# Kernel tuning notes

Measured on AMD Instinct MI355X. Metric: run time of the kernel, lower is better.

Reference implementation:

```python
import jax, jax.numpy as jnp
import numpy as np

B, T, D = 32, 512, 384
DUR_MAX = 8          # durations drawn from [0, DUR_MAX)
MAX_LEN = T * (DUR_MAX - 1)  # 3584, static pad length (= target_mel_len)


def setup_inputs() -> dict:
    key = jax.random.key(0)
    kx, kd = jax.random.split(key)
    x = jax.random.normal(kx, (B, T, D), dtype=jnp.float32)
    duration_target = jax.random.randint(kd, (B, T), 0, DUR_MAX, dtype=jnp.int64)
    return {"x": x, "duration_target": duration_target, "target_mel_len": MAX_LEN}


def reference(x, duration_target, target_mel_len):
    # Effective duration: original does vec.expand(max(int(d), 1), -1),
    # so zero durations still produce one frame.
    eff = jnp.maximum(duration_target, 1)          # [B, T]
    cum = jnp.cumsum(eff, axis=1)                   # [B, T] exclusive upper bounds
    mel_len = cum[:, -1]                            # [B]
    L = int(target_mel_len)                         # static pad length
    frames = jnp.arange(L)                          # [L]
    # frame j belongs to phoneme i where cum[i-1] <= j < cum[i]
    idx = jax.vmap(lambda c: jnp.searchsorted(c, frames, side="right"))(cum)  # [B, L]
    idx = jnp.minimum(idx, x.shape[1] - 1)          # clamp padded region
    out = jnp.take_along_axis(x, idx[:, :, None], axis=1)  # [B, L, D]
    mask = frames[None, :] < mel_len[:, None]       # [B, L]
    out = out * mask[:, :, None].astype(out.dtype)  # zero padding like F.pad
    return out, mel_len.astype(jnp.int64)
```

## Files before the change

### kernel.cpp

```cpp
#include <hip/hip_runtime.h>


#define B_DIM 32
#define T_DIM 512
#define D_DIM 384
#define L_DIM 3584
#define VEC_PER_ROW 96
#define PAIRS_PER_BATCH (L_DIM * VEC_PER_ROW / 2)
#define GATHER_BLOCK 256
#define BLOCKS_PER_BATCH (PAIRS_PER_BATCH / GATHER_BLOCK)
#define GATHER_BLOCKS (BLOCKS_PER_BATCH * B_DIM)

typedef float f32x4 __attribute__((ext_vector_type(4)));

__global__ void __launch_bounds__(T_DIM)
lr_build_map(const int* __restrict__ dur, int* __restrict__ idx_map,
             float* __restrict__ mel_out) {
    const int b    = blockIdx.x;
    const int t    = threadIdx.x;
    const int lane = t & 63;
    const int wv   = t >> 6;

    int d = dur[b * T_DIM + t];
    int e = d > 1 ? d : 1;

    int val = e;
    #pragma unroll
    for (int off = 1; off < 64; off <<= 1) {
        int n = __shfl_up(val, off, 64);
        if (lane >= off) val += n;
    }

    __shared__ int wsum[8];
    if (lane == 63) wsum[wv] = val;
    __syncthreads();

    int base = 0, tot = 0;
    #pragma unroll
    for (int i = 0; i < 8; ++i) {
        int s = wsum[i];
        tot += s;
        if (i < wv) base += s;
    }

    const int cum   = val + base;
    const int mel   = tot;
    const int start = cum - e;

    int* map_b = idx_map + b * L_DIM;
    for (int k = 0; k < e; ++k)
        map_b[start + k] = t;

    for (int f = mel + t; f < L_DIM; f += T_DIM)
        map_b[f] = -1;

    if (t == 0)
        mel_out[b] = (float)mel;
}

__global__ void __launch_bounds__(GATHER_BLOCK)
lr_gather(const f32x4* __restrict__ x, const int* __restrict__ idx_map,
          f32x4* __restrict__ out) {
    const int bid = blockIdx.x;
    const int blk = (bid & 7) * (GATHER_BLOCKS / 8) + (bid >> 3);

    const int b    = blk / BLOCKS_PER_BATCH;
    const int pblk = blk - b * BLOCKS_PER_BATCH;
    const int p    = pblk * GATHER_BLOCK + threadIdx.x;
    const int v0   = p << 1;
    const int f    = v0 / VEC_PER_ROW;
    const int w    = v0 - f * VEC_PER_ROW;

    const int idx = idx_map[b * L_DIM + f];
    f32x4 a = (f32x4)0.f;
    f32x4 c = (f32x4)0.f;
    if (idx >= 0) {
        const f32x4* row = x + ((b * T_DIM + idx) * VEC_PER_ROW);
        a = row[w];
        c = row[w + 1];
    }
    f32x4* o = out + (size_t)(b * L_DIM + f) * VEC_PER_ROW + w;
    __builtin_nontemporal_store(a, o);
    __builtin_nontemporal_store(c, o + 1);
}

extern "C" void kernel_launch(void* const* d_in, const int* in_sizes, int n_in,
                              void* d_out, int out_size, void* d_ws, size_t ws_size,
                              hipStream_t stream) {
    const float* x   = (const float*)d_in[0];
    const int*   dur = (const int*)d_in[1];

    int*   idx_map = (int*)d_ws;
    float* out     = (float*)d_out;
    float* mel_out = out + (size_t)B_DIM * L_DIM * D_DIM;

    lr_build_map<<<dim3(B_DIM), dim3(T_DIM), 0, stream>>>(dur, idx_map, mel_out);

    lr_gather<<<dim3(GATHER_BLOCKS), dim3(GATHER_BLOCK), 0, stream>>>(
        (const f32x4*)x, idx_map, (f32x4*)out);
}
```

Measured before the change: 221.8 us.

## Replace per-frame gather with per-phoneme scatter from LDS-staged rows

The scan kernel now only writes cumulative durations instead of building a full frame-to-phoneme index map. The write kernel has each block load 8 source rows of x into LDS once and write out every frame those rows cover, finding the owning row with seven comparisons. Separate blocks zero-fill the padded tail past mel_len. This removes the index-map writes and reads and the repeated global reads of x, at the cost of uneven per-block work and no longer using nontemporal stores.

```diff
diff --git a/kernel.cpp b/kernel.cpp
--- a/kernel.cpp
+++ b/kernel.cpp
@@ -5,17 +5,21 @@
 #define T_DIM 512
 #define D_DIM 384
 #define L_DIM 3584
-#define VEC_PER_ROW 96
-#define PAIRS_PER_BATCH (L_DIM * VEC_PER_ROW / 2)
-#define GATHER_BLOCK 256
-#define BLOCKS_PER_BATCH (PAIRS_PER_BATCH / GATHER_BLOCK)
-#define GATHER_BLOCKS (BLOCKS_PER_BATCH * B_DIM)
+#define VEC 96
+#define RPB 8
+#define CHUNKS (T_DIM / RPB)
+#define SCATTER_BLOCKS (B_DIM * CHUNKS)
+#define TAIL_F0 T_DIM
+#define TAIL_FPB 256
+#define TAIL_CHUNKS ((L_DIM - TAIL_F0) / TAIL_FPB)
+#define TAIL_BLOCKS (B_DIM * TAIL_CHUNKS)
+#define TOTAL_BLOCKS (SCATTER_BLOCKS + TAIL_BLOCKS)
 
 typedef float f32x4 __attribute__((ext_vector_type(4)));
 
 __global__ void __launch_bounds__(T_DIM)
-lr_build_map(const int* __restrict__ dur, int* __restrict__ idx_map,
-             float* __restrict__ mel_out) {
+lr_scan(const int* __restrict__ dur, int* __restrict__ cum_out,
+        float* __restrict__ mel_out) {
     const int b    = blockIdx.x;
     const int t    = threadIdx.x;
     const int lane = t & 63;
@@ -43,45 +47,64 @@
         if (i < wv) base += s;
     }
 
-    const int cum   = val + base;
-    const int mel   = tot;
-    const int start = cum - e;
-
-    int* map_b = idx_map + b * L_DIM;
-    for (int k = 0; k < e; ++k)
-        map_b[start + k] = t;
-
-    for (int f = mel + t; f < L_DIM; f += T_DIM)
-        map_b[f] = -1;
-
-    if (t == 0)
-        mel_out[b] = (float)mel;
+    cum_out[b * T_DIM + t] = val + base;
+    if (t == 0) mel_out[b] = (float)tot;
 }
 
-__global__ void __launch_bounds__(GATHER_BLOCK)
-lr_gather(const f32x4* __restrict__ x, const int* __restrict__ idx_map,
-          f32x4* __restrict__ out) {
-    const int bid = blockIdx.x;
-    const int blk = (bid & 7) * (GATHER_BLOCKS / 8) + (bid >> 3);
+__global__ void __launch_bounds__(256)
+lr_write(const f32x4* __restrict__ x, const int* __restrict__ cum,
+         f32x4* __restrict__ out) {
+    const int blk = blockIdx.x;
+    const int tid = threadIdx.x;
 
-    const int b    = blk / BLOCKS_PER_BATCH;
-    const int pblk = blk - b * BLOCKS_PER_BATCH;
-    const int p    = pblk * GATHER_BLOCK + threadIdx.x;
-    const int v0   = p << 1;
-    const int f    = v0 / VEC_PER_ROW;
-    const int w    = v0 - f * VEC_PER_ROW;
+    if (blk < SCATTER_BLOCKS) {
+        const int b  = blk / CHUNKS;
+        const int c  = blk - b * CHUNKS;
+        const int r0 = c * RPB;
 
-    const int idx = idx_map[b * L_DIM + f];
-    f32x4 a = (f32x4)0.f;
-    f32x4 c = (f32x4)0.f;
-    if (idx >= 0) {
-        const f32x4* row = x + ((b * T_DIM + idx) * VEC_PER_ROW);
-        a = row[w];
-        c = row[w + 1];
+        __shared__ f32x4 lx[RPB * VEC];
+        __shared__ int   scum[RPB + 1];
+
+        if (tid <= RPB) {
+            int r = r0 - 1 + tid;
+            scum[tid] = (r < 0) ? 0 : cum[b * T_DIM + r];
+        }
+        const f32x4* xb = x + (b * T_DIM + r0) * VEC;
+        #pragma unroll
+        for (int i = 0; i < (RPB * VEC) / 256; ++i)
+            lx[tid + i * 256] = xb[tid + i * 256];
+        __syncthreads();
+
+        const int f0 = scum[0];
+        const int s1 = scum[1], s2 = scum[2], s3 = scum[3], s4 = scum[4],
+                  s5 = scum[5], s6 = scum[6], s7 = scum[7];
+        const int span = (scum[RPB] - f0) * VEC;
+
+        f32x4* ob = out + (size_t)(b * L_DIM + f0) * VEC;
+        for (int v = tid; v < span; v += 256) {
+            const int fr = v / VEC;
+            const int w  = v - fr * VEC;
+            const int fa = f0 + fr;
+            int r = (fa >= s1) + (fa >= s2) + (fa >= s3) + (fa >= s4)
+                  + (fa >= s5) + (fa >= s6) + (fa >= s7);
+            ob[v] = lx[r * VEC + w];
+        }
+    } else {
+        const int tb = blk - SCATTER_BLOCKS;
+        const int b  = tb / TAIL_CHUNKS;
+        const int c  = tb - b * TAIL_CHUNKS;
+        const int mel = cum[b * T_DIM + T_DIM - 1];
+        const int fs = TAIL_F0 + c * TAIL_FPB;
+        const int lo = fs > mel ? fs : mel;
+        const int hi = fs + TAIL_FPB;
+        if (lo < hi) {
+            const f32x4 z = (f32x4)0.f;
+            f32x4* ob = out + (size_t)(b * L_DIM + lo) * VEC;
+            const int span = (hi - lo) * VEC;
+            for (int v = tid; v < span; v += 256)
+                ob[v] = z;
+        }
     }
-    f32x4* o = out + (size_t)(b * L_DIM + f) * VEC_PER_ROW + w;
-    __builtin_nontemporal_store(a, o);
-    __builtin_nontemporal_store(c, o + 1);
 }
 
 extern "C" void kernel_launch(void* const* d_in, const int* in_sizes, int n_in,
@@ -90,12 +113,12 @@
     const float* x   = (const float*)d_in[0];
     const int*   dur = (const int*)d_in[1];
 
-    int*   idx_map = (int*)d_ws;
+    int*   cum     = (int*)d_ws;
     float* out     = (float*)d_out;
     float* mel_out = out + (size_t)B_DIM * L_DIM * D_DIM;
 
-    lr_build_map<<<dim3(B_DIM), dim3(T_DIM), 0, stream>>>(dur, idx_map, mel_out);
+    lr_scan<<<dim3(B_DIM), dim3(T_DIM), 0, stream>>>(dur, cum, mel_out);
 
-    lr_gather<<<dim3(GATHER_BLOCKS), dim3(GATHER_BLOCK), 0, stream>>>(
-        (const f32x4*)x, idx_map, (f32x4*)out);
+    lr_write<<<dim3(TOTAL_BLOCKS), dim3(256), 0, stream>>>(
+        (const f32x4*)x, cum, (f32x4*)out);
 }
```

Result: faster. 195.6 us (-11.8%).

## Fuse map build and gather into single scatter kernel with per-block prefix scan

Applied to the files above, without the earlier changes.

Replaces the two-kernel approach (build an index map in workspace, then gather per output frame) with one kernel. Each block redoes the duration prefix scan for its batch in shared memory, loads 8 input rows once, and writes each row repeatedly to its output frames. Blocks also split the padded tail and zero it. This removes a launch, the index-map round trip and the repeated reads of x. In exchange the scan is repeated 64 times per batch, writes vary in length per thread, and the non-temporal stores are dropped.

```diff
diff --git a/kernel.cpp b/kernel.cpp
--- a/kernel.cpp
+++ b/kernel.cpp
@@ -5,83 +5,83 @@
 #define T_DIM 512
 #define D_DIM 384
 #define L_DIM 3584
-#define VEC_PER_ROW 96
-#define PAIRS_PER_BATCH (L_DIM * VEC_PER_ROW / 2)
-#define GATHER_BLOCK 256
-#define BLOCKS_PER_BATCH (PAIRS_PER_BATCH / GATHER_BLOCK)
-#define GATHER_BLOCKS (BLOCKS_PER_BATCH * B_DIM)
+#define VEC 96
+#define RPB 8
+#define CHUNKS (T_DIM / RPB)
+#define BLOCKS (B_DIM * CHUNKS)
 
 typedef float f32x4 __attribute__((ext_vector_type(4)));
 
-__global__ void __launch_bounds__(T_DIM)
-lr_build_map(const int* __restrict__ dur, int* __restrict__ idx_map,
-             float* __restrict__ mel_out) {
-    const int b    = blockIdx.x;
+__global__ void __launch_bounds__(256)
+lr_fused(const f32x4* __restrict__ x, const int* __restrict__ dur,
+         f32x4* __restrict__ out, float* __restrict__ mel_out) {
+    const int blk  = blockIdx.x;
+    const int b    = blk >> 6;
+    const int c    = blk & 63;
     const int t    = threadIdx.x;
     const int lane = t & 63;
     const int wv   = t >> 6;
 
-    int d = dur[b * T_DIM + t];
-    int e = d > 1 ? d : 1;
+    const int2 dd = ((const int2*)(dur + b * T_DIM))[t];
+    const int e0 = dd.x > 1 ? dd.x : 1;
+    const int e1 = dd.y > 1 ? dd.y : 1;
 
-    int val = e;
+    int val = e0 + e1;
     #pragma unroll
     for (int off = 1; off < 64; off <<= 1) {
         int n = __shfl_up(val, off, 64);
         if (lane >= off) val += n;
     }
 
-    __shared__ int wsum[8];
+    __shared__ int wsum[4];
+    __shared__ int scum[T_DIM];
     if (lane == 63) wsum[wv] = val;
     __syncthreads();
 
     int base = 0, tot = 0;
     #pragma unroll
-    for (int i = 0; i < 8; ++i) {
-        int s = wsum[i];
-        tot += s;
-        if (i < wv) base += s;
+    for (int i = 0; i < 4; ++i) {
+        int w = wsum[i];
+        tot += w;
+        if (i < wv) base += w;
+    }
+    const int c1 = val + base;
+    scum[2 * t]     = c1 - e1;
+    scum[2 * t + 1] = c1;
+    __syncthreads();
+
+    const int mel = tot;
+    if (c == 0 && t == 0)
+        mel_out[b] = (float)mel;
+
+    const int r0 = c * RPB;
+    const f32x4* xb   = x + (size_t)(b * T_DIM + r0) * VEC;
+    f32x4*       outb = out + (size_t)b * L_DIM * VEC;
+
+    #pragma unroll
+    for (int i = 0; i < 3; ++i) {
+        const int v = t + i * 256;
+        const int r = v / VEC;
+        const int w = v - r * VEC;
+        const f32x4 xv = xb[v];
+        const int gr = r0 + r;
+        const int ce = scum[gr];
+        const int cs = (gr == 0) ? 0 : scum[gr - 1];
+        f32x4* o = outb + (size_t)cs * VEC + w;
+        for (int k = cs; k < ce; ++k) {
+            *o = xv;
+            o += VEC;
+        }
     }
 
-    const int cum   = val + base;
-    const int mel   = tot;
-    const int start = cum - e;
-
-    int* map_b = idx_map + b * L_DIM;
-    for (int k = 0; k < e; ++k)
-        map_b[start + k] = t;
-
-    for (int f = mel + t; f < L_DIM; f += T_DIM)
-        map_b[f] = -1;
-
-    if (t == 0)
-        mel_out[b] = (float)mel;
-}
-
-__global__ void __launch_bounds__(GATHER_BLOCK)
-lr_gather(const f32x4* __restrict__ x, const int* __restrict__ idx_map,
-          f32x4* __restrict__ out) {
-    const int bid = blockIdx.x;
-    const int blk = (bid & 7) * (GATHER_BLOCKS / 8) + (bid >> 3);
-
-    const int b    = blk / BLOCKS_PER_BATCH;
-    const int pblk = blk - b * BLOCKS_PER_BATCH;
-    const int p    = pblk * GATHER_BLOCK + threadIdx.x;
-    const int v0   = p << 1;
-    const int f    = v0 / VEC_PER_ROW;
-    const int w    = v0 - f * VEC_PER_ROW;
-
-    const int idx = idx_map[b * L_DIM + f];
-    f32x4 a = (f32x4)0.f;
-    f32x4 c = (f32x4)0.f;
-    if (idx >= 0) {
-        const f32x4* row = x + ((b * T_DIM + idx) * VEC_PER_ROW);
-        a = row[w];
-        c = row[w + 1];
-    }
-    f32x4* o = out + (size_t)(b * L_DIM + f) * VEC_PER_ROW + w;
-    __builtin_nontemporal_store(a, o);
-    __builtin_nontemporal_store(c, o + 1);
+    const int tailspan = L_DIM - mel;
+    const int lo = mel + ((tailspan * c) >> 6);
+    const int hi = mel + ((tailspan * (c + 1)) >> 6);
+    const int n4 = (hi - lo) * VEC;
+    const f32x4 z = (f32x4)0.f;
+    f32x4* ob = outb + (size_t)lo * VEC;
+    for (int v = t; v < n4; v += 256)
+        ob[v] = z;
 }
 
 extern "C" void kernel_launch(void* const* d_in, const int* in_sizes, int n_in,
@@ -90,12 +90,9 @@
     const float* x   = (const float*)d_in[0];
     const int*   dur = (const int*)d_in[1];
 
-    int*   idx_map = (int*)d_ws;
     float* out     = (float*)d_out;
     float* mel_out = out + (size_t)B_DIM * L_DIM * D_DIM;
 
-    lr_build_map<<<dim3(B_DIM), dim3(T_DIM), 0, stream>>>(dur, idx_map, mel_out);
-
-    lr_gather<<<dim3(GATHER_BLOCKS), dim3(GATHER_BLOCK), 0, stream>>>(
-        (const f32x4*)x, idx_map, (f32x4*)out);
+    lr_fused<<<dim3(BLOCKS), dim3(256), 0, stream>>>(
+        (const f32x4*)x, dur, (f32x4*)out, mel_out);
 }
```

Result: faster. 193.5 us (-12.8%).
